# Performance work log

Hardware: AMD Instinct MI355X
Metric: run time of the kernel (lower is better)

The kernel has to match this reference:

```python
import jax, jax.numpy as jnp
import numpy as np
from jax import lax

B, C, H, W = 10, 3, 50, 101

# write order within one fill(): 9 neighbors (0.5) in nested-loop order, then center (1.0)
_OFF = jnp.array([[-1, -1], [-1, 0], [-1, 1], [0, -1], [0, 0], [0, 1], [1, -1], [1, 0], [1, 1], [0, 0]], dtype=jnp.int32)


def build_grid(x):
    """Faithful last-write-wins replay of the python-loop scatter.
    x: [B, C, K, 2] int, (col, row) pairs. Returns [B, C, H, W] float32."""
    Bc, Cc, K, _ = x.shape
    # fill(t, i, j, 48, 50) happens first for every (i, j): prepend point (col=50, row=48)
    base = jnp.broadcast_to(jnp.array([50, 48], dtype=x.dtype), (Bc, Cc, 1, 2))
    pts = jnp.concatenate([base, x], axis=2)            # [B, C, K+1, 2]
    K1 = K + 1
    rows = pts[..., 1][..., None] + _OFF[:, 0]          # [B, C, K1, 10]
    cols = pts[..., 0][..., None] + _OFF[:, 1]
    i = jnp.arange(Bc, dtype=jnp.int32)[:, None, None, None]
    j = jnp.arange(Cc, dtype=jnp.int32)[None, :, None, None]
    cell = ((i * Cc + j) * H + rows) * W + cols         # flat grid index per write
    # sequential write order within each (i, j) slice; slices never collide
    order = jnp.arange(K1, dtype=jnp.int32)[:, None] * 10 + jnp.arange(10, dtype=jnp.int32)[None, :]
    order = jnp.broadcast_to(order, cell.shape)
    last = jax.ops.segment_max(order.reshape(-1), cell.reshape(-1), num_segments=Bc * Cc * H * W)
    touched = last >= 0                                 # untouched cells get iinfo(int32).min
    val = jnp.where(last % 10 == 9, 1.0, 0.5)           # last write was a center (1.0) or neighbor (0.5)
    grid = jnp.where(touched, val, 0.0).astype(jnp.float32)
    return grid.reshape(Bc, Cc, H, W)


def conv2d(x, w, b, stride, pad):
    y = lax.conv_general_dilated(x, w, (stride, stride), [(pad, pad), (pad, pad)],
                                 dimension_numbers=('NCHW', 'OIHW', 'NCHW'))
    return y + b[None, :, None, None]


def maxpool(x, k, s):
    return lax.reduce_window(x, -jnp.inf, lax.max, (1, 1, k, k), (1, 1, s, s), 'VALID')


def net(grid, w1, b1, w2, b2, w3, b3, wl1, bl1, wl2, bl2):
    h = maxpool(jax.nn.relu(conv2d(grid, w1, b1, 2, 3)), 3, 2)   # [B,32,12,25]
    h = maxpool(jax.nn.relu(conv2d(h, w2, b2, 1, 2)), 2, 2)      # [B,64,6,12]
    h = maxpool(jax.nn.relu(conv2d(h, w3, b3, 1, 1)), 2, 2)      # [B,128,3,6]
    h = jnp.mean(h, axis=(2, 3))                                 # AdaptiveAvgPool2d(1,1) + Flatten
    h = jax.nn.relu(h @ wl1.T + bl1)
    return h @ wl2.T + bl2


def setup_inputs() -> dict:
    key = jax.random.key(0)
    ks = jax.random.split(key, 12)
    K = 4096
    cols = jax.random.randint(ks[0], (B, C, K, 1), 1, 100, dtype=jnp.int32)
    rows = jax.random.randint(ks[1], (B, C, K, 1), 1, 49, dtype=jnp.int32)
    x = jnp.concatenate([cols, rows], axis=-1)  # (col, row) pairs as in b__[0], b__[1]
    def rn(k, shape, fan_in):
        return jax.random.normal(k, shape, dtype=jnp.float32) * (1.0 / np.sqrt(fan_in))
    return {
        'x': x,
        'w1': rn(ks[2], (32, 3, 7, 7), 3 * 49), 'b1': rn(ks[3], (32,), 32),
        'w2': rn(ks[4], (64, 32, 5, 5), 32 * 25), 'b2': rn(ks[5], (64,), 64),
        'w3': rn(ks[6], (128, 64, 3, 3), 64 * 9), 'b3': rn(ks[7], (128,), 128),
        'wl1': rn(ks[8], (128, 128), 128), 'bl1': rn(ks[9], (128,), 128),
        'wl2': rn(ks[10], (5, 128), 128), 'bl2': rn(ks[11], (5,), 128),
    }


def reference(x, w1, b1, w2, b2, w3, b3, wl1, bl1, wl2, bl2):
    grid = build_grid(x)
    return net(grid, w1, b1, w2, b2, w3, b3, wl1, bl1, wl2, bl2)
```

## Files before the change

kernel.cpp:

```cpp
#include <hip/hip_runtime.h>

#define Bb 10
#define Hh 50
#define Ww 101
#define Kk 4096
#define SLICE (Hh*Ww)


__global__ __launch_bounds__(1024) void scatter_grid_kernel(
        const int* __restrict__ x, float* __restrict__ grid, unsigned* __restrict__ cnt) {
    __shared__ int lastKp[52 * 104];
    __shared__ int rowm[52 * 104];
    int bc = blockIdx.x;
    int tid = threadIdx.x;
    if (bc < Bb && tid == 0)
        __hip_atomic_store(&cnt[bc], 0u, __ATOMIC_RELEASE, __HIP_MEMORY_SCOPE_AGENT);
    for (int i = tid; i < 52 * 104; i += 1024) lastKp[i] = -1;
    __syncthreads();
    const int2* xp = (const int2*)(x + bc * Kk * 2);
    for (int k = tid; k < Kk + 1; k += 1024) {
        int col, row;
        if (k == 0) { col = 50; row = 48; }
        else { int2 p = xp[k - 1]; col = p.x; row = p.y; }
        atomicMax(&lastKp[(row + 1) * 104 + (col + 1)], k);
    }
    __syncthreads();
    for (int i = tid; i < 52 * 101; i += 1024) {
        int r = i / 101, c = i % 101 + 1;
        const int* lp = &lastKp[r * 104 + c];
        rowm[r * 104 + c] = max(max(lp[-1], lp[0]), lp[1]);
    }
    __syncthreads();
    float* g = grid + bc * SLICE;
    for (int i = tid; i < SLICE; i += 1024) {
        int r = i / Ww + 1, c = i % Ww + 1;
        int M = max(max(rowm[(r - 1) * 104 + c], rowm[r * 104 + c]),
                    rowm[(r + 1) * 104 + c]);
        g[i] = (M < 0) ? 0.0f : ((lastKp[r * 104 + c] == M) ? 1.0f : 0.5f);
    }
}

__global__ __launch_bounds__(256) void conv1p1_kernel(
        const float* __restrict__ grid, const float* __restrict__ w1,
        const float* __restrict__ b1, float* __restrict__ p1) {
    __shared__ float tile[3 * 15 * 109];
    __shared__ float w1s[4 * 3 * 49];
    __shared__ float ctile[4 * 5 * 52];
    int blk = blockIdx.x;
    int b = blk / 48, rem48 = blk % 48;
    int ocq = rem48 / 6, phb = rem48 % 6;
    int oc0 = ocq * 4;
    int tid = threadIdx.x;
    int row0 = 8 * phb - 3;

    for (int i = tid; i < 588; i += 256) w1s[i] = w1[oc0 * 147 + i];
    for (int i = tid; i < 3 * 15 * 109; i += 256) {
        int ic = i / 1635, rem = i % 1635;
        int r = rem / 109, c = rem % 109;
        int gr = row0 + r, gc = c - 3;
        float v = 0.f;
        if (gr >= 0 && gr < Hh && gc >= 0 && gc < Ww)
            v = grid[((b * 3 + ic) * Hh + gr) * Ww + gc];
        tile[i] = v;
    }
    __syncthreads();
    for (int t = tid; t < 260; t += 256) {
        int oc_l = t / 65, rem = t % 65;
        int r_l = rem / 13, quad = rem % 13;
        int ow0 = quad * 4;
        float acc[4] = {0.f, 0.f, 0.f, 0.f};
        for (int ic = 0; ic < 3; ++ic) {
            const float* wp = w1s + (oc_l * 3 + ic) * 49;
            const float* tp = tile + ic * 1635 + (2 * r_l) * 109 + 8 * quad;
            #pragma unroll
            for (int kh = 0; kh < 7; ++kh) {
                const float* lr = tp + kh * 109;
                float s[13];
                #pragma unroll
                for (int k = 0; k < 13; ++k) s[k] = lr[k];
                float wa[7];
                #pragma unroll
                for (int k = 0; k < 7; ++k) wa[k] = wp[kh * 7 + k];
                #pragma unroll
                for (int kw = 0; kw < 7; ++kw)
                    #pragma unroll
                    for (int j = 0; j < 4; ++j)
                        acc[j] += s[2 * j + kw] * wa[kw];
            }
        }
        float bia = b1[oc0 + oc_l];
        #pragma unroll
        for (int j = 0; j < 4; ++j) {
            int ow = ow0 + j;
            if (ow < 51)
                ctile[(oc_l * 5 + r_l) * 52 + ow] = fmaxf(acc[j] + bia, 0.f);
        }
    }
    __syncthreads();
    if (tid < 200) {
        int oc_l = tid / 50, rem = tid % 50;
        int ph_l = rem / 25, pw = rem % 25;
        const float* cp = ctile + (oc_l * 5 + 2 * ph_l) * 52 + 2 * pw;
        float m = -INFINITY;
        #pragma unroll
        for (int r = 0; r < 3; ++r)
            #pragma unroll
            for (int c = 0; c < 3; ++c)
                m = fmaxf(m, cp[r * 52 + c]);
        int ph = 2 * phb + ph_l;
        p1[((b * 32 + oc0 + oc_l) * 12 + ph) * 25 + pw] = m;
    }
}

__global__ __launch_bounds__(1024) void conv2p2_kernel(
        const float* __restrict__ p1, const float* __restrict__ w2,
        const float* __restrict__ b2, float* __restrict__ p2) {
    __shared__ float lds[32 * 16 * 29];
    __shared__ float part[256 * 4];
    int blk = blockIdx.x;
    int b = blk / 18;
    int tid = threadIdx.x;
    for (int i = tid; i < 32 * 16 * 29; i += 1024) {
        int ic = i / 464, rem = i % 464;
        int r = rem / 29, c = rem % 29;
        int gr = r - 2, gc = c - 2;
        float v = 0.f;
        if (gr >= 0 && gr < 12 && gc >= 0 && gc < 25)
            v = p1[((b * 32 + ic) * 12 + gr) * 25 + gc];
        lds[i] = v;
    }
    __syncthreads();
    int u_l = tid & 255, q = tid >> 8;
    int u = (blk % 18) * 256 + u_l;
    int pw = u % 12, ph = (u / 12) % 6, oc = u / 72;
    float acc[2][2] = {{0.f, 0.f}, {0.f, 0.f}};
    const float* wbase = w2 + oc * 32 * 25;
    const float* lbase = lds + (2 * ph) * 29 + 2 * pw;
    int ic0 = q * 8;
    for (int ic = ic0; ic < ic0 + 8; ++ic) {
        float inr[6][6];
        const float* lp = lbase + ic * 464;
        #pragma unroll
        for (int r = 0; r < 6; ++r)
            #pragma unroll
            for (int c = 0; c < 6; ++c)
                inr[r][c] = lp[r * 29 + c];
        const float* wp = wbase + ic * 25;
        float wr[25];
        #pragma unroll
        for (int k = 0; k < 25; ++k) wr[k] = wp[k];
        #pragma unroll
        for (int kh = 0; kh < 5; ++kh)
            #pragma unroll
            for (int kw = 0; kw < 5; ++kw)
                #pragma unroll
                for (int dy = 0; dy < 2; ++dy)
                    #pragma unroll
                    for (int dx = 0; dx < 2; ++dx)
                        acc[dy][dx] += inr[dy + kh][dx + kw] * wr[kh * 5 + kw];
    }
    #pragma unroll
    for (int src = 1; src < 4; ++src) {
        if (q == src) {
            #pragma unroll
            for (int dy = 0; dy < 2; ++dy)
                #pragma unroll
                for (int dx = 0; dx < 2; ++dx)
                    part[u_l * 4 + dy * 2 + dx] = acc[dy][dx];
        }
        __syncthreads();
        if (q == 0) {
            #pragma unroll
            for (int dy = 0; dy < 2; ++dy)
                #pragma unroll
                for (int dx = 0; dx < 2; ++dx)
                    acc[dy][dx] += part[u_l * 4 + dy * 2 + dx];
        }
        if (src < 3) __syncthreads();
    }
    if (q == 0) {
        float bia = b2[oc];
        float m = fmaxf(fmaxf(fmaxf(acc[0][0], acc[0][1]),
                              fmaxf(acc[1][0], acc[1][1])) + bia, 0.f);
        p2[((b * 64 + oc) * 6 + ph) * 12 + pw] = m;
    }
}

__global__ __launch_bounds__(1024) void conv3p3_head_kernel(
        const float* __restrict__ p2, const float* __restrict__ w3,
        const float* __restrict__ b3, float* __restrict__ featbuf,
        unsigned* __restrict__ cnt,
        const float* __restrict__ wl1, const float* __restrict__ bl1,
        const float* __restrict__ wl2, const float* __restrict__ bl2,
        float* __restrict__ out) {
    __shared__ float smf[64 * 8 * 14];
    __shared__ float part[144 * 4];
    __shared__ float red[144];
    __shared__ unsigned lastflag;
    int blk = blockIdx.x;
    int b = blk / 16, blk16 = blk % 16;
    int tid = threadIdx.x;
    for (int i = tid; i < 64 * 8 * 14; i += 1024) {
        int ic = i / 112, rem = i % 112;
        int r = rem / 14, c = rem % 14;
        int gr = r - 1, gc = c - 1;
        float v = 0.f;
        if (gr >= 0 && gr < 6 && gc >= 0 && gc < 12)
            v = p2[((b * 64 + ic) * 6 + gr) * 12 + gc];
        smf[i] = v;
    }
    __syncthreads();
    int lid = tid & 255, q = tid >> 8;
    float acc[2][2] = {{0.f, 0.f}, {0.f, 0.f}};
    int u = blk16 * 144 + lid;
    int pw = u % 6, ph = (u / 6) % 3, oc = u / 18;
    if (lid < 144) {
        const float* wbase = w3 + oc * 64 * 9;
        const float* lbase = smf + (2 * ph) * 14 + 2 * pw;
        int ic0 = q * 16;
        for (int ic = ic0; ic < ic0 + 16; ++ic) {
            float inr[4][4];
            const float* lp = lbase + ic * 112;
            #pragma unroll
            for (int r = 0; r < 4; ++r)
                #pragma unroll
                for (int c = 0; c < 4; ++c)
                    inr[r][c] = lp[r * 14 + c];
            const float* wp = wbase + ic * 9;
            float wr[9];
            #pragma unroll
            for (int k = 0; k < 9; ++k) wr[k] = wp[k];
            #pragma unroll
            for (int kh = 0; kh < 3; ++kh)
                #pragma unroll
                for (int kw = 0; kw < 3; ++kw)
                    #pragma unroll
                    for (int dy = 0; dy < 2; ++dy)
                        #pragma unroll
                        for (int dx = 0; dx < 2; ++dx)
                            acc[dy][dx] += inr[dy + kh][dx + kw] * wr[kh * 3 + kw];
        }
    }
    #pragma unroll
    for (int src = 1; src < 4; ++src) {
        if (q == src && lid < 144) {
            #pragma unroll
            for (int dy = 0; dy < 2; ++dy)
                #pragma unroll
                for (int dx = 0; dx < 2; ++dx)
                    part[lid * 4 + dy * 2 + dx] = acc[dy][dx];
        }
        __syncthreads();
        if (q == 0 && lid < 144) {
            #pragma unroll
            for (int dy = 0; dy < 2; ++dy)
                #pragma unroll
                for (int dx = 0; dx < 2; ++dx)
                    acc[dy][dx] += part[lid * 4 + dy * 2 + dx];
        }
        if (src < 3) __syncthreads();
    }
    if (q == 0 && lid < 144) {
        float bia = b3[oc];
        red[lid] = fmaxf(fmaxf(fmaxf(acc[0][0], acc[0][1]),
                               fmaxf(acc[1][0], acc[1][1])) + bia, 0.f);
    }
    __syncthreads();
    if (tid < 8) {
        float s = 0.0f;
        #pragma unroll
        for (int k = 0; k < 18; ++k) s += red[tid * 18 + k];
        __hip_atomic_store(&featbuf[b * 128 + blk16 * 8 + tid], s * (1.0f / 18.0f),
                           __ATOMIC_RELEASE, __HIP_MEMORY_SCOPE_AGENT);
    }
    __syncthreads();
    if (tid == 0) {
        unsigned prev = __hip_atomic_fetch_add(&cnt[b], 1u, __ATOMIC_ACQ_REL,
                                               __HIP_MEMORY_SCOPE_AGENT);
        lastflag = (prev == 15u) ? 1u : 0u;
    }
    __syncthreads();
    if (lastflag) {
        float* feat = smf;
        float* h2 = smf + 128;
        int c = tid;
        if (c < 128)
            feat[c] = __hip_atomic_load(&featbuf[b * 128 + c],
                                        __ATOMIC_ACQUIRE, __HIP_MEMORY_SCOPE_AGENT);
        __syncthreads();
        if (c < 128) {
            float a = bl1[c];
            const float4* wr = (const float4*)(wl1 + c * 128);
            #pragma unroll 8
            for (int k4 = 0; k4 < 32; ++k4) {
                float4 w = wr[k4];
                a += feat[4 * k4] * w.x + feat[4 * k4 + 1] * w.y
                   + feat[4 * k4 + 2] * w.z + feat[4 * k4 + 3] * w.w;
            }
            h2[c] = fmaxf(a, 0.0f);
        }
        __syncthreads();
        if (c < 5) {
            float a2 = bl2[c];
            const float4* wr2 = (const float4*)(wl2 + c * 128);
            #pragma unroll 8
            for (int k4 = 0; k4 < 32; ++k4) {
                float4 w = wr2[k4];
                a2 += h2[4 * k4] * w.x + h2[4 * k4 + 1] * w.y
                    + h2[4 * k4 + 2] * w.z + h2[4 * k4 + 3] * w.w;
            }
            out[b * 5 + c] = a2;
        }
    }
}

extern "C" void kernel_launch(void* const* d_in, const int* in_sizes, int n_in,
                              void* d_out, int out_size, void* d_ws, size_t ws_size,
                              hipStream_t stream) {
    const int*   x   = (const int*)d_in[0];
    const float* w1  = (const float*)d_in[1];
    const float* b1  = (const float*)d_in[2];
    const float* w2  = (const float*)d_in[3];
    const float* b2  = (const float*)d_in[4];
    const float* w3  = (const float*)d_in[5];
    const float* b3  = (const float*)d_in[6];
    const float* wl1 = (const float*)d_in[7];
    const float* bl1 = (const float*)d_in[8];
    const float* wl2 = (const float*)d_in[9];
    const float* bl2 = (const float*)d_in[10];
    float* out = (float*)d_out;

    char* ws = (char*)d_ws;
    float*    grid    = (float*)ws;
    float*    p1      = (float*)(ws + 606000);
    float*    p2g     = (float*)(ws + 990000);
    float*    featbuf = (float*)(ws + 1174320);
    unsigned* cnt     = (unsigned*)(ws + 1179440);

    scatter_grid_kernel<<<30, 1024, 0, stream>>>(x, grid, cnt);
    conv1p1_kernel<<<480, 256, 0, stream>>>(grid, w1, b1, p1);
    conv2p2_kernel<<<180, 1024, 0, stream>>>(p1, w2, b2, p2g);
    conv3p3_head_kernel<<<160, 1024, 0, stream>>>(p2g, w3, b3, featbuf, cnt,
                                                  wl1, bl1, wl2, bl2, out);
}
```

Baseline: 72.77 us.

## Widen intra-block channel split and single-pass partial reductions across conv kernels

conv2 now splits output rows across two blocks per batch (360 blocks) and divides input channels into eight groups of four instead of four groups of eight, reducing all partials with one barrier. conv3 uses seven channel groups of 144 threads instead of four groups of 256 with 112 idle lanes, again reducing in one pass. conv1 uses 512-thread blocks so the tile load is spread over more threads and the 260 compute threads run in a single pass. The aim is more parallelism and fewer serialized barriers, at the cost of more shared memory for partials and extra halo loads in conv2.

```diff
diff --git a/kernel.cpp b/kernel.cpp
--- a/kernel.cpp
+++ b/kernel.cpp
@@ -40,7 +40,7 @@
     }
 }
 
-__global__ __launch_bounds__(256) void conv1p1_kernel(
+__global__ __launch_bounds__(512) void conv1p1_kernel(
         const float* __restrict__ grid, const float* __restrict__ w1,
         const float* __restrict__ b1, float* __restrict__ p1) {
     __shared__ float tile[3 * 15 * 109];
@@ -53,8 +53,8 @@
     int tid = threadIdx.x;
     int row0 = 8 * phb - 3;
 
-    for (int i = tid; i < 588; i += 256) w1s[i] = w1[oc0 * 147 + i];
-    for (int i = tid; i < 3 * 15 * 109; i += 256) {
+    for (int i = tid; i < 588; i += 512) w1s[i] = w1[oc0 * 147 + i];
+    for (int i = tid; i < 3 * 15 * 109; i += 512) {
         int ic = i / 1635, rem = i % 1635;
         int r = rem / 109, c = rem % 109;
         int gr = row0 + r, gc = c - 3;
@@ -64,7 +64,8 @@
         tile[i] = v;
     }
     __syncthreads();
-    for (int t = tid; t < 260; t += 256) {
+    if (tid < 260) {
+        int t = tid;
         int oc_l = t / 65, rem = t % 65;
         int r_l = rem / 13, quad = rem % 13;
         int ow0 = quad * 4;
@@ -115,31 +116,32 @@
 __global__ __launch_bounds__(1024) void conv2p2_kernel(
         const float* __restrict__ p1, const float* __restrict__ w2,
         const float* __restrict__ b2, float* __restrict__ p2) {
-    __shared__ float lds[32 * 16 * 29];
-    __shared__ float part[256 * 4];
+    __shared__ float lds2[32 * 10 * 29];
+    __shared__ float part[7 * 128 * 4];
     int blk = blockIdx.x;
-    int b = blk / 18;
+    int b = blk / 36, rem36 = blk % 36;
+    int sh = rem36 / 18, blkl = rem36 % 18;
     int tid = threadIdx.x;
-    for (int i = tid; i < 32 * 16 * 29; i += 1024) {
-        int ic = i / 464, rem = i % 464;
-        int r = rem / 29, c = rem % 29;
-        int gr = r - 2, gc = c - 2;
+    for (int i = tid; i < 32 * 10 * 29; i += 1024) {
+        int ic = i / 290, rem = i % 290;
+        int pr_l = rem / 29, c = rem % 29;
+        int gr = 6 * sh + pr_l - 2, gc = c - 2;
         float v = 0.f;
         if (gr >= 0 && gr < 12 && gc >= 0 && gc < 25)
             v = p1[((b * 32 + ic) * 12 + gr) * 25 + gc];
-        lds[i] = v;
-    }
-    __syncthreads();
-    int u_l = tid & 255, q = tid >> 8;
-    int u = (blk % 18) * 256 + u_l;
-    int pw = u % 12, ph = (u / 12) % 6, oc = u / 72;
+        lds2[i] = v;
+    }
+    __syncthreads();
+    int lid = tid & 127, q = tid >> 7;
+    int u = blkl * 128 + lid;
+    int pw = u % 12, ph_l = (u / 12) % 3, oc = u / 36;
     float acc[2][2] = {{0.f, 0.f}, {0.f, 0.f}};
     const float* wbase = w2 + oc * 32 * 25;
-    const float* lbase = lds + (2 * ph) * 29 + 2 * pw;
-    int ic0 = q * 8;
-    for (int ic = ic0; ic < ic0 + 8; ++ic) {
+    const float* lbase = lds2 + (2 * ph_l) * 29 + 2 * pw;
+    int ic0 = q * 4;
+    for (int ic = ic0; ic < ic0 + 4; ++ic) {
         float inr[6][6];
-        const float* lp = lbase + ic * 464;
+        const float* lp = lbase + ic * 290;
         #pragma unroll
         for (int r = 0; r < 6; ++r)
             #pragma unroll
@@ -159,29 +161,26 @@
                     for (int dx = 0; dx < 2; ++dx)
                         acc[dy][dx] += inr[dy + kh][dx + kw] * wr[kh * 5 + kw];
     }
-    #pragma unroll
-    for (int src = 1; src < 4; ++src) {
-        if (q == src) {
+    if (q > 0) {
+        #pragma unroll
+        for (int dy = 0; dy < 2; ++dy)
+            #pragma unroll
+            for (int dx = 0; dx < 2; ++dx)
+                part[((q - 1) * 128 + lid) * 4 + dy * 2 + dx] = acc[dy][dx];
+    }
+    __syncthreads();
+    if (q == 0) {
+        #pragma unroll
+        for (int src = 0; src < 7; ++src)
             #pragma unroll
             for (int dy = 0; dy < 2; ++dy)
                 #pragma unroll
                 for (int dx = 0; dx < 2; ++dx)
-                    part[u_l * 4 + dy * 2 + dx] = acc[dy][dx];
-        }
-        __syncthreads();
-        if (q == 0) {
-            #pragma unroll
-            for (int dy = 0; dy < 2; ++dy)
-                #pragma unroll
-                for (int dx = 0; dx < 2; ++dx)
-                    acc[dy][dx] += part[u_l * 4 + dy * 2 + dx];
-        }
-        if (src < 3) __syncthreads();
-    }
-    if (q == 0) {
+                    acc[dy][dx] += part[(src * 128 + lid) * 4 + dy * 2 + dx];
         float bia = b2[oc];
         float m = fmaxf(fmaxf(fmaxf(acc[0][0], acc[0][1]),
                               fmaxf(acc[1][0], acc[1][1])) + bia, 0.f);
+        int ph = 3 * sh + ph_l;
         p2[((b * 64 + oc) * 6 + ph) * 12 + pw] = m;
     }
 }
@@ -194,7 +193,7 @@
         const float* __restrict__ wl2, const float* __restrict__ bl2,
         float* __restrict__ out) {
     __shared__ float smf[64 * 8 * 14];
-    __shared__ float part[144 * 4];
+    __shared__ float part[6 * 144 * 4];
     __shared__ float red[144];
     __shared__ unsigned lastflag;
     int blk = blockIdx.x;
@@ -210,15 +209,17 @@
         smf[i] = v;
     }
     __syncthreads();
-    int lid = tid & 255, q = tid >> 8;
+    int q = tid / 144, lid = tid % 144;
+    bool act = q < 7;
     float acc[2][2] = {{0.f, 0.f}, {0.f, 0.f}};
     int u = blk16 * 144 + lid;
     int pw = u % 6, ph = (u / 6) % 3, oc = u / 18;
-    if (lid < 144) {
+    if (act) {
         const float* wbase = w3 + oc * 64 * 9;
         const float* lbase = smf + (2 * ph) * 14 + 2 * pw;
-        int ic0 = q * 16;
-        for (int ic = ic0; ic < ic0 + 16; ++ic) {
+        int ic0 = q * 9;
+        int ic1 = (q == 6) ? 64 : ic0 + 9;
+        for (int ic = ic0; ic < ic1; ++ic) {
             float inr[4][4];
             const float* lp = lbase + ic * 112;
             #pragma unroll
@@ -240,27 +241,23 @@
                         for (int dx = 0; dx < 2; ++dx)
                             acc[dy][dx] += inr[dy + kh][dx + kw] * wr[kh * 3 + kw];
         }
-    }
-    #pragma unroll
-    for (int src = 1; src < 4; ++src) {
-        if (q == src && lid < 144) {
+        if (q > 0) {
             #pragma unroll
             for (int dy = 0; dy < 2; ++dy)
                 #pragma unroll
                 for (int dx = 0; dx < 2; ++dx)
-                    part[lid * 4 + dy * 2 + dx] = acc[dy][dx];
-        }
-        __syncthreads();
-        if (q == 0 && lid < 144) {
+                    part[((q - 1) * 144 + lid) * 4 + dy * 2 + dx] = acc[dy][dx];
+        }
+    }
+    __syncthreads();
+    if (q == 0) {
+        #pragma unroll
+        for (int src = 0; src < 6; ++src)
             #pragma unroll
             for (int dy = 0; dy < 2; ++dy)
                 #pragma unroll
                 for (int dx = 0; dx < 2; ++dx)
-                    acc[dy][dx] += part[lid * 4 + dy * 2 + dx];
-        }
-        if (src < 3) __syncthreads();
-    }
-    if (q == 0 && lid < 144) {
+                    acc[dy][dx] += part[(src * 144 + lid) * 4 + dy * 2 + dx];
         float bia = b3[oc];
         red[lid] = fmaxf(fmaxf(fmaxf(acc[0][0], acc[0][1]),
                                fmaxf(acc[1][0], acc[1][1])) + bia, 0.f);
@@ -338,8 +335,8 @@
     unsigned* cnt     = (unsigned*)(ws + 1179440);
 
     scatter_grid_kernel<<<30, 1024, 0, stream>>>(x, grid, cnt);
-    conv1p1_kernel<<<480, 256, 0, stream>>>(grid, w1, b1, p1);
-    conv2p2_kernel<<<180, 1024, 0, stream>>>(p1, w2, b2, p2g);
+    conv1p1_kernel<<<480, 512, 0, stream>>>(grid, w1, b1, p1);
+    conv2p2_kernel<<<360, 1024, 0, stream>>>(p1, w2, b2, p2g);
     conv3p3_head_kernel<<<160, 1024, 0, stream>>>(p2g, w3, b3, featbuf, cnt,
                                                   wl1, bl1, wl2, bl2, out);
 }
```

Result: faster. 64.16 us (-11.8%).
